# Kernel tuning notes

Measured on AMD Instinct MI355X. Metric: run time of the kernel, lower is better.

## Reference

```python
import jax, jax.numpy as jnp
import numpy as np

BATCH = 32768
D = 256       # input_dim
N = 4096      # n_features
K = 32        # top-k


def setup_inputs() -> dict:
    key = jax.random.key(0)
    k_x, k_we, k_wd = jax.random.split(key, 3)
    x = jax.random.normal(k_x, (BATCH, D), dtype=jnp.float32)
    # kaiming-uniform-like init, then unit-norm decoder columns (as in __init__)
    bound_e = float(np.sqrt(6.0 / D))
    W_enc = jax.random.uniform(k_we, (N, D), jnp.float32, -bound_e, bound_e)
    bound_d = float(np.sqrt(6.0 / N))
    W_dec = jax.random.uniform(k_wd, (D, N), jnp.float32, -bound_d, bound_d)
    W_dec = W_dec / jnp.linalg.norm(W_dec, axis=0, keepdims=True)
    return {
        "x": x,
        "W_enc": W_enc,
        "b_enc": jnp.zeros((N,), jnp.float32),
        "W_dec": W_dec,
        "b_dec": jnp.zeros((D,), jnp.float32),
        "input_mean": jnp.zeros((D,), jnp.float32),
        "input_std": jnp.ones((D,), jnp.float32),
    }


def reference(x, W_enc, b_enc, W_dec, b_dec, input_mean, input_std):
    # normalize -> center by decoder bias -> encode
    x_norm = (x - input_mean) / input_std                      # (B, D)
    x_centered = x_norm - b_dec                                # (B, D)
    h_pre = jnp.einsum('bd,nd->bn', x_centered, W_enc) + b_enc  # (B, N)

    # top-k mask: keep K largest entries per row (values * binary mask)
    _, topk_idx = jax.lax.top_k(h_pre, K)                      # (B, K)
    rows = jnp.arange(h_pre.shape[0])[:, None]                 # (B, 1)
    mask = jnp.zeros_like(h_pre).at[rows, topk_idx].set(1.0)
    h_sparse = h_pre * mask                                    # (B, N)

    # decode in normalized space
    x_hat_norm = jnp.einsum('bn,dn->bd', h_sparse, W_dec) + b_dec  # (B, D)
    return (x_hat_norm, h_sparse, h_pre)
```

## Files before the change

kernel.cpp:

```cpp
#include <hip/hip_runtime.h>
#include <stdint.h>

#define BATCH 32768
#define DIM   256
#define NFEAT 4096
#define KTOP  32

__device__ __forceinline__ uint32_t f2u(float f) {
    uint32_t b = __float_as_uint(f);
    return (b & 0x80000000u) ? ~b : (b | 0x80000000u);
}
__device__ __forceinline__ float u2f(uint32_t u) {
    uint32_t b = (u & 0x80000000u) ? (u ^ 0x80000000u) : ~u;
    return __uint_as_float(b);
}

__global__ __launch_bounds__(256) void prep_xc(const float* __restrict__ x,
                                               const float* __restrict__ mean,
                                               const float* __restrict__ stdv,
                                               const float* __restrict__ b_dec,
                                               float* __restrict__ xc) {
    int g = blockIdx.x * 256 + threadIdx.x;
    int d0 = (g * 4) & (DIM - 1);
    float4 xv = ((const float4*)x)[g];
    float4 mv = *(const float4*)&mean[d0];
    float4 sv = *(const float4*)&stdv[d0];
    float4 bv = *(const float4*)&b_dec[d0];
    float4 o;
    o.x = (xv.x - mv.x) / sv.x - bv.x;
    o.y = (xv.y - mv.y) / sv.y - bv.y;
    o.z = (xv.z - mv.z) / sv.z - bv.z;
    o.w = (xv.w - mv.w) / sv.w - bv.w;
    ((float4*)xc)[g] = o;
}

__global__ __launch_bounds__(256) void transpose_wdec(const float* __restrict__ wd,
                                                      float* __restrict__ wdt) {
    __shared__ float t[32][33];
    int bx = blockIdx.x;
    int by = blockIdx.y;
    int lx = threadIdx.x & 31, ly = threadIdx.x >> 5;
#pragma unroll
    for (int i = 0; i < 4; i++) {
        int d = by * 32 + ly + i * 8;
        t[ly + i * 8][lx] = wd[(size_t)d * NFEAT + bx * 32 + lx];
    }
    __syncthreads();
#pragma unroll
    for (int i = 0; i < 4; i++) {
        int n = bx * 32 + ly + i * 8;
        wdt[(size_t)n * DIM + by * 32 + lx] = t[lx][ly + i * 8];
    }
}

__global__ __launch_bounds__(256) void encode_gemm(const float* __restrict__ A,
                                                   const float* __restrict__ W,
                                                   const float* __restrict__ be,
                                                   float* __restrict__ hpre) {
    __shared__ float As[8][128];
    __shared__ float Bs[8][128];
    int bx = blockIdx.x;
    int by = blockIdx.y;
    int tid = threadIdx.x;
    int row0 = by * 128, col0 = bx * 128;

    int ar = tid >> 1;
    int ac = (tid & 1) * 4;
    const float* Ap = A + (size_t)(row0 + ar) * DIM + ac;
    const float* Wp = W + (size_t)(col0 + ar) * DIM + ac;

    int tx = tid & 15, ty = tid >> 4;

    float acc[8][8];
#pragma unroll
    for (int i = 0; i < 8; i++)
#pragma unroll
        for (int j = 0; j < 8; j++) acc[i][j] = 0.0f;

    for (int ko = 0; ko < DIM; ko += 8) {
        float4 av = *(const float4*)(Ap + ko);
        float4 wv = *(const float4*)(Wp + ko);
        __syncthreads();
        As[ac + 0][ar] = av.x; As[ac + 1][ar] = av.y;
        As[ac + 2][ar] = av.z; As[ac + 3][ar] = av.w;
        Bs[ac + 0][ar] = wv.x; Bs[ac + 1][ar] = wv.y;
        Bs[ac + 2][ar] = wv.z; Bs[ac + 3][ar] = wv.w;
        __syncthreads();
#pragma unroll
        for (int kk = 0; kk < 8; kk++) {
            float a[8], b[8];
            *(float4*)(a)     = *(const float4*)&As[kk][ty * 8];
            *(float4*)(a + 4) = *(const float4*)&As[kk][ty * 8 + 4];
            *(float4*)(b)     = *(const float4*)&Bs[kk][tx * 8];
            *(float4*)(b + 4) = *(const float4*)&Bs[kk][tx * 8 + 4];
#pragma unroll
            for (int i = 0; i < 8; i++)
#pragma unroll
                for (int j = 0; j < 8; j++) acc[i][j] += a[i] * b[j];
        }
    }

    float bev[8];
#pragma unroll
    for (int j = 0; j < 8; j++) bev[j] = be[col0 + tx * 8 + j];
#pragma unroll
    for (int i = 0; i < 8; i++) {
        int r = row0 + ty * 8 + i;
        float4 o0, o1;
        o0.x = acc[i][0] + bev[0]; o0.y = acc[i][1] + bev[1];
        o0.z = acc[i][2] + bev[2]; o0.w = acc[i][3] + bev[3];
        o1.x = acc[i][4] + bev[4]; o1.y = acc[i][5] + bev[5];
        o1.z = acc[i][6] + bev[6]; o1.w = acc[i][7] + bev[7];
        float* op = hpre + (size_t)r * NFEAT + col0 + tx * 8;
        *(float4*)op = o0;
        *(float4*)(op + 4) = o1;
    }
}

__global__ __launch_bounds__(256) void topk_decode(const float* __restrict__ hpre,
                                                   const float* __restrict__ wdt,
                                                   const float* __restrict__ b_dec,
                                                   float* __restrict__ hsp,
                                                   float* __restrict__ xhat) {
    int row = blockIdx.x;
    int tid = threadIdx.x;
    __shared__ uint32_t hist[256];
    __shared__ uint32_t sfx[257];
    __shared__ float cval[KTOP];
    __shared__ int   cidx[KTOP];
    __shared__ int   eqidx[64];
    __shared__ int   ccnt, eqcnt, selBin;

    uint32_t uu[16];
    const float* rp = hpre + (size_t)row * NFEAT;
#pragma unroll
    for (int i = 0; i < 16; i++) uu[i] = f2u(rp[i * 256 + tid]);

    uint32_t pref = 0;
    int kRem = KTOP;
    for (int p = 0; p < 4; p++) {
        int shift = 24 - 8 * p;
        hist[tid] = 0;
        __syncthreads();
#pragma unroll
        for (int i = 0; i < 16; i++) {
            uint32_t u = uu[i];
            bool ok = (p == 0) || ((u >> (shift + 8)) == pref);
            if (ok) atomicAdd(&hist[(u >> shift) & 255u], 1u);
        }
        __syncthreads();
        sfx[tid] = hist[tid];
        if (tid == 0) sfx[256] = 0;
        __syncthreads();
        for (int off = 1; off < 256; off <<= 1) {
            uint32_t v = (tid + off < 256) ? sfx[tid + off] : 0u;
            __syncthreads();
            sfx[tid] += v;
            __syncthreads();
        }
        if (sfx[tid] >= (uint32_t)kRem && sfx[tid + 1] < (uint32_t)kRem) selBin = tid;
        __syncthreads();
        int sb = selBin;
        kRem -= (int)sfx[sb + 1];
        pref = (pref << 8) | (uint32_t)sb;
        __syncthreads();
    }

    if (tid == 0) { ccnt = 0; eqcnt = 0; }
    __syncthreads();

    float* hrow = hsp + (size_t)row * NFEAT;
#pragma unroll
    for (int i = 0; i < 16; i++) {
        int n = i * 256 + tid;
        uint32_t u = uu[i];
        float w = 0.0f;
        if (u > pref) {
            int s = atomicAdd(&ccnt, 1);
            float f = u2f(u);
            cval[s] = f; cidx[s] = n;
            w = f;
        } else if (u == pref) {
            int e = atomicAdd(&eqcnt, 1);
            if (e < 64) eqidx[e] = n;
        }
        hrow[n] = w;
    }
    __syncthreads();

    if (tid == 0) {
        int e = eqcnt; if (e > 64) e = 64;
        for (int a = 1; a < e; a++) {
            int v = eqidx[a]; int b2 = a - 1;
            while (b2 >= 0 && eqidx[b2] > v) { eqidx[b2 + 1] = eqidx[b2]; b2--; }
            eqidx[b2 + 1] = v;
        }
        int base = ccnt;
        float thrf = u2f(pref);
        for (int j = 0; j < kRem && j < e && (base + j) < KTOP; j++) {
            int n = eqidx[j];
            cidx[base + j] = n; cval[base + j] = thrf;
            hrow[n] = thrf;
        }
    }
    __syncthreads();

    float accv = b_dec[tid];
#pragma unroll 8
    for (int k2 = 0; k2 < KTOP; k2++) {
        accv += cval[k2] * wdt[(size_t)cidx[k2] * DIM + tid];
    }
    xhat[(size_t)row * DIM + tid] = accv;
}

extern "C" void kernel_launch(void* const* d_in, const int* in_sizes, int n_in,
                              void* d_out, int out_size, void* d_ws, size_t ws_size,
                              hipStream_t stream) {
    const float* x     = (const float*)d_in[0];
    const float* W_enc = (const float*)d_in[1];
    const float* b_enc = (const float*)d_in[2];
    const float* W_dec = (const float*)d_in[3];
    const float* b_dec = (const float*)d_in[4];
    const float* mean  = (const float*)d_in[5];
    const float* stdv  = (const float*)d_in[6];

    float* out  = (float*)d_out;
    float* xhat = out;
    float* hsp  = out + (size_t)BATCH * DIM;
    float* hpre = hsp + (size_t)BATCH * NFEAT;

    float* xc  = (float*)d_ws;
    float* wdt = xc + (size_t)BATCH * DIM;

    prep_xc<<<(BATCH * DIM) / 1024, 256, 0, stream>>>(x, mean, stdv, b_dec, xc);
    transpose_wdec<<<dim3(NFEAT / 32, DIM / 32), 256, 0, stream>>>(W_dec, wdt);
    encode_gemm<<<dim3(NFEAT / 128, BATCH / 128), 256, 0, stream>>>(xc, W_enc, b_enc, hpre);
    topk_decode<<<BATCH, 256, 0, stream>>>(hpre, wdt, b_dec, hsp, xhat);
}
```

Baseline: 2.047 ms.

## Use split-bf16 MFMA encode GEMM and wave-per-row top-k with fp32 rescoring

The encoder GEMM now runs on bf16 MFMA instructions. Each fp32 operand is split into hi and lo bf16 halves, and three partial products (hi·hi, hi·lo, lo·hi) approximate fp32 accuracy. Tiles are staged through LDS with direct global-to-LDS loads and blocks are swizzled for locality. Top-k moves to one wavefront per row: a 32-step bisection picks 40 candidates, their scores are recomputed exactly in fp32 from W_enc, a bitonic sort keeps the top 32, and the decode uses float4 loads. The aim is to replace the slow scalar-FMA GEMM and the block-wide radix select. The cost is three split prep passes and a risk that h_pre differs slightly from fp32, which could change the top-k set or ordering.

After: 2.398 ms. 1.17x slower.

```diff
diff --git a/kernel.cpp b/kernel.cpp
--- a/kernel.cpp
+++ b/kernel.cpp
@@ -5,40 +5,92 @@
 #define DIM   256
 #define NFEAT 4096
 #define KTOP  32
+#define KSPL  512
+#define RSEL  40
+
+typedef __attribute__((ext_vector_type(8))) short bf16x8;
+typedef __attribute__((ext_vector_type(4))) float f32x4;
 
 __device__ __forceinline__ uint32_t f2u(float f) {
     uint32_t b = __float_as_uint(f);
     return (b & 0x80000000u) ? ~b : (b | 0x80000000u);
 }
-__device__ __forceinline__ float u2f(uint32_t u) {
-    uint32_t b = (u & 0x80000000u) ? (u ^ 0x80000000u) : ~u;
-    return __uint_as_float(b);
-}
-
-__global__ __launch_bounds__(256) void prep_xc(const float* __restrict__ x,
-                                               const float* __restrict__ mean,
-                                               const float* __restrict__ stdv,
-                                               const float* __restrict__ b_dec,
-                                               float* __restrict__ xc) {
+
+__device__ __forceinline__ ushort f2bf_rne(float f) {
+    uint32_t u = __float_as_uint(f);
+    uint32_t lsb = (u >> 16) & 1u;
+    u += 0x7fffu + lsb;
+    return (ushort)(u >> 16);
+}
+__device__ __forceinline__ float bf2f(ushort s) {
+    return __uint_as_float(((uint32_t)s) << 16);
+}
+
+__device__ __forceinline__ void gload_lds16(const void* gsrc, void* ldsdst) {
+    __builtin_amdgcn_global_load_lds(
+        (const __attribute__((address_space(1))) uint32_t*)(uintptr_t)gsrc,
+        (__attribute__((address_space(3))) uint32_t*)(uint32_t)(uintptr_t)ldsdst,
+        16, 0, 0);
+}
+
+__global__ __launch_bounds__(256) void prep_a_split(const float* __restrict__ x,
+                                                    const float* __restrict__ mean,
+                                                    const float* __restrict__ stdv,
+                                                    const float* __restrict__ bdec,
+                                                    ushort* __restrict__ Asp) {
     int g = blockIdx.x * 256 + threadIdx.x;
-    int d0 = (g * 4) & (DIM - 1);
+    int b = g >> 6;
+    int q = g & 63;
     float4 xv = ((const float4*)x)[g];
-    float4 mv = *(const float4*)&mean[d0];
-    float4 sv = *(const float4*)&stdv[d0];
-    float4 bv = *(const float4*)&b_dec[d0];
-    float4 o;
-    o.x = (xv.x - mv.x) / sv.x - bv.x;
-    o.y = (xv.y - mv.y) / sv.y - bv.y;
-    o.z = (xv.z - mv.z) / sv.z - bv.z;
-    o.w = (xv.w - mv.w) / sv.w - bv.w;
-    ((float4*)xc)[g] = o;
+    float4 mv = ((const float4*)mean)[q];
+    float4 sv = ((const float4*)stdv)[q];
+    float4 bv = ((const float4*)bdec)[q];
+    float c[4];
+    c[0] = (xv.x - mv.x) / sv.x - bv.x;
+    c[1] = (xv.y - mv.y) / sv.y - bv.y;
+    c[2] = (xv.z - mv.z) / sv.z - bv.z;
+    c[3] = (xv.w - mv.w) / sv.w - bv.w;
+    ushort h0[4], h1[4];
+#pragma unroll
+    for (int j = 0; j < 4; j++) {
+        h0[j] = f2bf_rne(c[j]);
+        h1[j] = f2bf_rne(c[j] - bf2f(h0[j]));
+    }
+    uint2 s0 = { (uint32_t)h0[0] | ((uint32_t)h0[1] << 16),
+                 (uint32_t)h0[2] | ((uint32_t)h0[3] << 16) };
+    uint2 s1 = { (uint32_t)h1[0] | ((uint32_t)h1[1] << 16),
+                 (uint32_t)h1[2] | ((uint32_t)h1[3] << 16) };
+    int d0 = q * 4;
+    *(uint2*)&Asp[(size_t)b * KSPL + d0]       = s0;
+    *(uint2*)&Asp[(size_t)b * KSPL + 256 + d0] = s1;
+}
+
+__global__ __launch_bounds__(256) void prep_b_split(const float* __restrict__ w,
+                                                    ushort* __restrict__ Bsp) {
+    int g = blockIdx.x * 256 + threadIdx.x;
+    int n = g >> 6;
+    int q = g & 63;
+    float4 wv = ((const float4*)w)[g];
+    float c[4] = { wv.x, wv.y, wv.z, wv.w };
+    ushort h0[4], h1[4];
+#pragma unroll
+    for (int j = 0; j < 4; j++) {
+        h0[j] = f2bf_rne(c[j]);
+        h1[j] = f2bf_rne(c[j] - bf2f(h0[j]));
+    }
+    uint2 s0 = { (uint32_t)h0[0] | ((uint32_t)h0[1] << 16),
+                 (uint32_t)h0[2] | ((uint32_t)h0[3] << 16) };
+    uint2 s1 = { (uint32_t)h1[0] | ((uint32_t)h1[1] << 16),
+                 (uint32_t)h1[2] | ((uint32_t)h1[3] << 16) };
+    int d0 = q * 4;
+    *(uint2*)&Bsp[(size_t)n * KSPL + d0]       = s0;
+    *(uint2*)&Bsp[(size_t)n * KSPL + 256 + d0] = s1;
 }
 
 __global__ __launch_bounds__(256) void transpose_wdec(const float* __restrict__ wd,
                                                       float* __restrict__ wdt) {
     __shared__ float t[32][33];
-    int bx = blockIdx.x;
-    int by = blockIdx.y;
+    int bx = blockIdx.x, by = blockIdx.y;
     int lx = threadIdx.x & 31, ly = threadIdx.x >> 5;
 #pragma unroll
     for (int i = 0; i < 4; i++) {
@@ -53,164 +105,202 @@
     }
 }
 
-__global__ __launch_bounds__(256) void encode_gemm(const float* __restrict__ A,
-                                                   const float* __restrict__ W,
+__global__ __launch_bounds__(256) void encode_gemm(const ushort* __restrict__ Asp,
+                                                   const ushort* __restrict__ Bsp,
                                                    const float* __restrict__ be,
                                                    float* __restrict__ hpre) {
-    __shared__ float As[8][128];
-    __shared__ float Bs[8][128];
-    int bx = blockIdx.x;
-    int by = blockIdx.y;
-    int tid = threadIdx.x;
-    int row0 = by * 128, col0 = bx * 128;
-
-    int ar = tid >> 1;
-    int ac = (tid & 1) * 4;
-    const float* Ap = A + (size_t)(row0 + ar) * DIM + ac;
-    const float* Wp = W + (size_t)(col0 + ar) * DIM + ac;
-
-    int tx = tid & 15, ty = tid >> 4;
-
-    float acc[8][8];
-#pragma unroll
-    for (int i = 0; i < 8; i++)
-#pragma unroll
-        for (int j = 0; j < 8; j++) acc[i][j] = 0.0f;
-
-    for (int ko = 0; ko < DIM; ko += 8) {
-        float4 av = *(const float4*)(Ap + ko);
-        float4 wv = *(const float4*)(Wp + ko);
-        __syncthreads();
-        As[ac + 0][ar] = av.x; As[ac + 1][ar] = av.y;
-        As[ac + 2][ar] = av.z; As[ac + 3][ar] = av.w;
-        Bs[ac + 0][ar] = wv.x; Bs[ac + 1][ar] = wv.y;
-        Bs[ac + 2][ar] = wv.z; Bs[ac + 3][ar] = wv.w;
-        __syncthreads();
-#pragma unroll
-        for (int kk = 0; kk < 8; kk++) {
-            float a[8], b[8];
-            *(float4*)(a)     = *(const float4*)&As[kk][ty * 8];
-            *(float4*)(a + 4) = *(const float4*)&As[kk][ty * 8 + 4];
-            *(float4*)(b)     = *(const float4*)&Bs[kk][tx * 8];
-            *(float4*)(b + 4) = *(const float4*)&Bs[kk][tx * 8 + 4];
-#pragma unroll
-            for (int i = 0; i < 8; i++)
-#pragma unroll
-                for (int j = 0; j < 8; j++) acc[i][j] += a[i] * b[j];
-        }
-    }
-
-    float bev[8];
-#pragma unroll
-    for (int j = 0; j < 8; j++) bev[j] = be[col0 + tx * 8 + j];
-#pragma unroll
-    for (int i = 0; i < 8; i++) {
-        int r = row0 + ty * 8 + i;
-        float4 o0, o1;
-        o0.x = acc[i][0] + bev[0]; o0.y = acc[i][1] + bev[1];
-        o0.z = acc[i][2] + bev[2]; o0.w = acc[i][3] + bev[3];
-        o1.x = acc[i][4] + bev[4]; o1.y = acc[i][5] + bev[5];
-        o1.z = acc[i][6] + bev[6]; o1.w = acc[i][7] + bev[7];
-        float* op = hpre + (size_t)r * NFEAT + col0 + tx * 8;
-        *(float4*)op = o0;
-        *(float4*)(op + 4) = o1;
+    __shared__ ushort smem[8192];
+    ushort* As = smem;
+    ushort* Bs = smem + 4096;
+
+    int bid = blockIdx.x;
+    int wg  = (bid & 7) * 1024 + (bid >> 3);
+    int nt  = wg & 31, mt = wg >> 5;
+    int row0 = mt * 128, col0 = nt * 128;
+
+    int t = threadIdx.x;
+    int lane = t & 63, w = t >> 6;
+    int wr = w >> 1, wc = w & 1;
+
+    int srow = t >> 2;
+    int scol = (t & 3) * 8;
+    const ushort* ga0 = Asp + (size_t)(row0 + srow) * KSPL + scol;
+    const ushort* ga1 = ga0 + (size_t)64 * KSPL;
+    const ushort* gb0 = Bsp + (size_t)(col0 + srow) * KSPL + scol;
+    const ushort* gb1 = gb0 + (size_t)64 * KSPL;
+    char* lA = (char*)As + t * 16;
+    char* lB = (char*)Bs + t * 16;
+
+    int aoff = ((wr * 64 + (lane & 15)) * 32 + (lane >> 4) * 8) * 2;
+    int boff = ((wc * 64 + (lane & 15)) * 32 + (lane >> 4) * 8) * 2;
+
+    f32x4 acc[4][4] = {};
+
+    for (int p = 0; p < 3; ++p) {
+        int kA = (p >> 1) * 256;
+        int kB = (p & 1) * 256;
+        for (int ko = 0; ko < 256; ko += 32) {
+            __syncthreads();
+            gload_lds16(ga0 + kA + ko, lA);
+            gload_lds16(ga1 + kA + ko, lA + 4096);
+            gload_lds16(gb0 + kB + ko, lB);
+            gload_lds16(gb1 + kB + ko, lB + 4096);
+            __syncthreads();
+            bf16x8 af[4], bf[4];
+#pragma unroll
+            for (int m = 0; m < 4; m++) af[m] = *(const bf16x8*)((char*)As + aoff + m * 1024);
+#pragma unroll
+            for (int n = 0; n < 4; n++) bf[n] = *(const bf16x8*)((char*)Bs + boff + n * 1024);
+#pragma unroll
+            for (int m = 0; m < 4; m++)
+#pragma unroll
+                for (int n = 0; n < 4; n++)
+                    acc[m][n] = __builtin_amdgcn_mfma_f32_16x16x32_bf16(af[m], bf[n], acc[m][n], 0, 0, 0);
+        }
+    }
+
+    int crow = row0 + wr * 64 + (lane >> 4) * 4;
+    int ccol = col0 + wc * 64 + (lane & 15);
+#pragma unroll
+    for (int n = 0; n < 4; n++) {
+        float bev = be[ccol + n * 16];
+#pragma unroll
+        for (int m = 0; m < 4; m++) {
+            float* op = hpre + (size_t)(crow + m * 16) * NFEAT + ccol + n * 16;
+#pragma unroll
+            for (int r = 0; r < 4; r++)
+                op[(size_t)r * NFEAT] = acc[m][n][r] + bev;
+        }
     }
 }
 
 __global__ __launch_bounds__(256) void topk_decode(const float* __restrict__ hpre,
+                                                   const float* __restrict__ x,
+                                                   const float* __restrict__ mean,
+                                                   const float* __restrict__ stdv,
+                                                   const float* __restrict__ bdec,
+                                                   const float* __restrict__ Wenc,
+                                                   const float* __restrict__ benc,
                                                    const float* __restrict__ wdt,
-                                                   const float* __restrict__ b_dec,
                                                    float* __restrict__ hsp,
                                                    float* __restrict__ xhat) {
-    int row = blockIdx.x;
-    int tid = threadIdx.x;
-    __shared__ uint32_t hist[256];
-    __shared__ uint32_t sfx[257];
-    __shared__ float cval[KTOP];
-    __shared__ int   cidx[KTOP];
-    __shared__ int   eqidx[64];
-    __shared__ int   ccnt, eqcnt, selBin;
-
-    uint32_t uu[16];
-    const float* rp = hpre + (size_t)row * NFEAT;
-#pragma unroll
-    for (int i = 0; i < 16; i++) uu[i] = f2u(rp[i * 256 + tid]);
-
-    uint32_t pref = 0;
-    int kRem = KTOP;
-    for (int p = 0; p < 4; p++) {
-        int shift = 24 - 8 * p;
-        hist[tid] = 0;
-        __syncthreads();
-#pragma unroll
-        for (int i = 0; i < 16; i++) {
-            uint32_t u = uu[i];
-            bool ok = (p == 0) || ((u >> (shift + 8)) == pref);
-            if (ok) atomicAdd(&hist[(u >> shift) & 255u], 1u);
-        }
-        __syncthreads();
-        sfx[tid] = hist[tid];
-        if (tid == 0) sfx[256] = 0;
-        __syncthreads();
-        for (int off = 1; off < 256; off <<= 1) {
-            uint32_t v = (tid + off < 256) ? sfx[tid + off] : 0u;
-            __syncthreads();
-            sfx[tid] += v;
-            __syncthreads();
-        }
-        if (sfx[tid] >= (uint32_t)kRem && sfx[tid + 1] < (uint32_t)kRem) selBin = tid;
-        __syncthreads();
-        int sb = selBin;
-        kRem -= (int)sfx[sb + 1];
-        pref = (pref << 8) | (uint32_t)sb;
-        __syncthreads();
-    }
-
-    if (tid == 0) { ccnt = 0; eqcnt = 0; }
-    __syncthreads();
-
-    float* hrow = hsp + (size_t)row * NFEAT;
-#pragma unroll
-    for (int i = 0; i < 16; i++) {
-        int n = i * 256 + tid;
-        uint32_t u = uu[i];
-        float w = 0.0f;
-        if (u > pref) {
-            int s = atomicAdd(&ccnt, 1);
-            float f = u2f(u);
-            cval[s] = f; cidx[s] = n;
-            w = f;
-        } else if (u == pref) {
-            int e = atomicAdd(&eqcnt, 1);
-            if (e < 64) eqidx[e] = n;
-        }
-        hrow[n] = w;
-    }
-    __syncthreads();
-
-    if (tid == 0) {
-        int e = eqcnt; if (e > 64) e = 64;
-        for (int a = 1; a < e; a++) {
-            int v = eqidx[a]; int b2 = a - 1;
-            while (b2 >= 0 && eqidx[b2] > v) { eqidx[b2 + 1] = eqidx[b2]; b2--; }
-            eqidx[b2 + 1] = v;
-        }
-        int base = ccnt;
-        float thrf = u2f(pref);
-        for (int j = 0; j < kRem && j < e && (base + j) < KTOP; j++) {
-            int n = eqidx[j];
-            cidx[base + j] = n; cval[base + j] = thrf;
-            hrow[n] = thrf;
-        }
-    }
-    __syncthreads();
-
-    float accv = b_dec[tid];
+    __shared__ float xcb[4][256];
+    __shared__ int   candn[4][64];
+    __shared__ float selv[4][32];
+    __shared__ int   seln[4][32];
+
+    int wv = threadIdx.x >> 6, lane = threadIdx.x & 63;
+    int row = blockIdx.x * 4 + wv;
+
+    {
+        float4 xv = ((const float4*)(x + (size_t)row * DIM))[lane];
+        float4 mv = ((const float4*)mean)[lane];
+        float4 sv = ((const float4*)stdv)[lane];
+        float4 bv = ((const float4*)bdec)[lane];
+        float4 o;
+        o.x = (xv.x - mv.x) / sv.x - bv.x;
+        o.y = (xv.y - mv.y) / sv.y - bv.y;
+        o.z = (xv.z - mv.z) / sv.z - bv.z;
+        o.w = (xv.w - mv.w) / sv.w - bv.w;
+        ((float4*)xcb[wv])[lane] = o;
+    }
+
+    uint32_t u[64];
+    const float4* hr = (const float4*)(hpre + (size_t)row * NFEAT);
+#pragma unroll
+    for (int c = 0; c < 16; c++) {
+        float4 v = hr[c * 64 + lane];
+        u[c * 4 + 0] = f2u(v.x);
+        u[c * 4 + 1] = f2u(v.y);
+        u[c * 4 + 2] = f2u(v.z);
+        u[c * 4 + 3] = f2u(v.w);
+    }
+
+    uint32_t lo = 0, hi = 0xFFFFFFFFu;
+    for (int it = 0; it < 32; ++it) {
+        uint32_t d = hi - lo;
+        uint32_t mid = lo + (d >> 1) + (d & 1);
+        int c = 0;
+#pragma unroll
+        for (int i = 0; i < 64; i++) c += (u[i] >= mid) ? 1 : 0;
+#pragma unroll
+        for (int off = 32; off; off >>= 1) c += __shfl_xor(c, off);
+        if (c >= RSEL) lo = mid; else hi = mid - 1;
+    }
+    uint32_t ustar = lo;
+
+    int base = 0;
+#pragma unroll
+    for (int c = 0; c < 16; c++) {
+#pragma unroll
+        for (int j = 0; j < 4; j++) {
+            bool pred = (u[c * 4 + j] >= ustar);
+            unsigned long long mask = __ballot(pred);
+            if (pred) {
+                int pos = base + __popcll(mask & ((1ull << lane) - 1ull));
+                if (pos < 64) candn[wv][pos] = c * 256 + lane * 4 + j;
+            }
+            base += __popcll(mask);
+        }
+    }
+    int ccnt = base < 64 ? base : 64;
+
+    float rv = -3.4e38f;
+    int   rn = 0x7FFFFFFF;
+    {
+        int n = (lane < ccnt) ? candn[wv][lane] : 0;
+        const float4* wr_ = (const float4*)(Wenc + (size_t)n * DIM);
+        const float4* xc4 = (const float4*)xcb[wv];
+        float s = 0.f;
 #pragma unroll 8
-    for (int k2 = 0; k2 < KTOP; k2++) {
-        accv += cval[k2] * wdt[(size_t)cidx[k2] * DIM + tid];
-    }
-    xhat[(size_t)row * DIM + tid] = accv;
+        for (int k = 0; k < 64; k++) {
+            float4 a = xc4[k];
+            float4 b = wr_[k];
+            s += a.x * b.x + a.y * b.y + a.z * b.z + a.w * b.w;
+        }
+        if (lane < ccnt) { rv = s + benc[n]; rn = n; }
+    }
+
+#pragma unroll
+    for (int k = 2; k <= 64; k <<= 1) {
+#pragma unroll
+        for (int j = k >> 1; j >= 1; j >>= 1) {
+            float ov = __shfl_xor(rv, j);
+            int   on = __shfl_xor(rn, j);
+            bool lower = (lane & j) == 0;
+            bool desc  = (lane & k) == 0;
+            bool mineBetter = (rv > ov) || (rv == ov && rn < on);
+            if ((lower == desc) != mineBetter) { rv = ov; rn = on; }
+        }
+    }
+    if (lane < KTOP) { selv[wv][lane] = rv; seln[wv][lane] = rn; }
+
+    float* ho = hsp + (size_t)row * NFEAT;
+#pragma unroll
+    for (int c = 0; c < 16; c++) {
+        float4 w4 = { 0.f, 0.f, 0.f, 0.f };
+#pragma unroll
+        for (int j = 0; j < 4; j++) {
+            if (u[c * 4 + j] >= ustar) {
+                int n = c * 256 + lane * 4 + j;
+                float val = 0.f;
+                for (int s = 0; s < KTOP; s++)
+                    if (seln[wv][s] == n) val = selv[wv][s];
+                ((float*)&w4)[j] = val;
+            }
+        }
+        ((float4*)ho)[c * 64 + lane] = w4;
+    }
+
+    float4 acc = ((const float4*)bdec)[lane];
+#pragma unroll 4
+    for (int s = 0; s < KTOP; s++) {
+        float v = selv[wv][s];
+        int   n = seln[wv][s];
+        float4 w4 = ((const float4*)(wdt + (size_t)n * DIM))[lane];
+        acc.x += v * w4.x; acc.y += v * w4.y; acc.z += v * w4.z; acc.w += v * w4.w;
+    }
+    ((float4*)(xhat + (size_t)row * DIM))[lane] = acc;
 }
 
 extern "C" void kernel_launch(void* const* d_in, const int* in_sizes, int n_in,
@@ -229,11 +319,14 @@
     float* hsp  = out + (size_t)BATCH * DIM;
     float* hpre = hsp + (size_t)BATCH * NFEAT;
 
-    float* xc  = (float*)d_ws;
-    float* wdt = xc + (size_t)BATCH * DIM;
-
-    prep_xc<<<(BATCH * DIM) / 1024, 256, 0, stream>>>(x, mean, stdv, b_dec, xc);
+    ushort* Asp = (ushort*)d_ws;
+    ushort* Bsp = Asp + (size_t)BATCH * KSPL;
+    float*  wdt = (float*)(Bsp + (size_t)NFEAT * KSPL);
+
+    prep_a_split<<<(BATCH * DIM / 4) / 256, 256, 0, stream>>>(x, mean, stdv, b_dec, Asp);
+    prep_b_split<<<(NFEAT * DIM / 4) / 256, 256, 0, stream>>>(W_enc, Bsp);
     transpose_wdec<<<dim3(NFEAT / 32, DIM / 32), 256, 0, stream>>>(W_dec, wdt);
-    encode_gemm<<<dim3(NFEAT / 128, BATCH / 128), 256, 0, stream>>>(xc, W_enc, b_enc, hpre);
-    topk_decode<<<BATCH, 256, 0, stream>>>(hpre, wdt, b_dec, hsp, xhat);
-}
+    encode_gemm<<<(BATCH / 128) * (NFEAT / 128), 256, 0, stream>>>(Asp, Bsp, b_enc, hpre);
+    topk_decode<<<BATCH / 4, 256, 0, stream>>>(hpre, x, mean, stdv, b_dec,
+                                               W_enc, b_enc, wdt, hsp, xhat);
+}
```
